# Kernel optimization log

Hardware: AMD Instinct MI355X
Metric: run time of the kernel (lower is better)

The kernel has to match this reference:

```python
import jax, jax.numpy as jnp
import numpy as np

D = 64          # node_hidden_dim
MP_STEPS = 6    # num_step_message_passing
S2S_STEPS = 6   # num_step_set2set
LSTM_LAYERS = 3 # num_layer_set2set


def setup_inputs() -> dict:
    key = jax.random.key(0)
    ks = jax.random.split(key, 32)
    N, E, B = 10000, 50000, 500
    node_in, edge_in, edge_hid, out_dim = 15, 5, 128, 12
    s = 0.1
    inp = {}
    inp["node_feat"] = jax.random.normal(ks[0], (N, node_in), jnp.float32)
    inp["edge_feat"] = jax.random.normal(ks[1], (E, edge_in), jnp.float32)
    inp["src"] = jax.random.randint(ks[2], (E,), 0, N)
    inp["dst"] = jax.random.randint(ks[3], (E,), 0, N)
    inp["graph_ids"] = jnp.sort(jax.random.randint(ks[4], (N,), 0, B))
    inp["num_graphs"] = B
    # lin0
    inp["lin0_W"] = jax.random.normal(ks[5], (node_in, D), jnp.float32) * s
    inp["lin0_b"] = jnp.zeros((D,), jnp.float32)
    # edge network MLP (Linear -> ReLU -> Linear), output reshaped to D x D per edge
    inp["em_W1"] = jax.random.normal(ks[6], (edge_in, edge_hid), jnp.float32) * s
    inp["em_b1"] = jnp.zeros((edge_hid,), jnp.float32)
    inp["em_W2"] = jax.random.normal(ks[7], (edge_hid, D * D), jnp.float32) * 0.02
    inp["em_b2"] = jnp.zeros((D * D,), jnp.float32)
    inp["conv_bias"] = jnp.zeros((D,), jnp.float32)
    # GRU (input D, hidden D), torch layout: [3*D, in], gate order r,z,n
    inp["gru_Wih"] = jax.random.normal(ks[8], (3 * D, D), jnp.float32) * s
    inp["gru_Whh"] = jax.random.normal(ks[9], (3 * D, D), jnp.float32) * s
    inp["gru_bih"] = jnp.zeros((3 * D,), jnp.float32)
    inp["gru_bhh"] = jnp.zeros((3 * D,), jnp.float32)
    # Set2Set LSTM: input 2*D, hidden D, 3 layers. torch layout [4*D, in], gates i,f,g,o
    inp["lstm0_Wih"] = jax.random.normal(ks[10], (4 * D, 2 * D), jnp.float32) * s
    inp["lstm0_Whh"] = jax.random.normal(ks[11], (4 * D, D), jnp.float32) * s
    inp["lstm0_bih"] = jnp.zeros((4 * D,), jnp.float32)
    inp["lstm0_bhh"] = jnp.zeros((4 * D,), jnp.float32)
    inp["lstm12_Wih"] = jax.random.normal(ks[12], (2, 4 * D, D), jnp.float32) * s
    inp["lstm12_Whh"] = jax.random.normal(ks[13], (2, 4 * D, D), jnp.float32) * s
    inp["lstm12_bih"] = jnp.zeros((2, 4 * D), jnp.float32)
    inp["lstm12_bhh"] = jnp.zeros((2, 4 * D), jnp.float32)
    # output head
    inp["lin1_W"] = jax.random.normal(ks[14], (2 * D, D), jnp.float32) * s
    inp["lin1_b"] = jnp.zeros((D,), jnp.float32)
    inp["lin2_W"] = jax.random.normal(ks[15], (D, out_dim), jnp.float32) * s
    inp["lin2_b"] = jnp.zeros((out_dim,), jnp.float32)
    return inp


def _mpnn(node_feat, edge_feat, src, dst, graph_ids, num_graphs,
          lin0_W, lin0_b, em_W1, em_b1, em_W2, em_b2, conv_bias,
          gru_Wih, gru_Whh, gru_bih, gru_bhh,
          lstm0_Wih, lstm0_Whh, lstm0_bih, lstm0_bhh,
          lstm12_Wih, lstm12_Whh, lstm12_bih, lstm12_bhh,
          lin1_W, lin1_b, lin2_W, lin2_b):
    N = node_feat.shape[0]
    E = edge_feat.shape[0]
    B = num_graphs
    # initial node embedding
    out = jax.nn.relu(node_feat @ lin0_W + lin0_b)      # [N, D]
    h = out                                             # GRU hidden (seq_len=1, 1 layer)
    # per-edge weight matrices (edge features are static across steps)
    We = (jax.nn.relu(edge_feat @ em_W1 + em_b1) @ em_W2 + em_b2).reshape(E, D, D)
    for _ in range(MP_STEPS):
        # NNConv: gather src -> per-edge matvec -> scatter-add to dst
        msg = jnp.einsum('ei,eio->eo', out[src], We)    # [E, D]
        agg = jax.ops.segment_sum(msg, dst, num_segments=N) + conv_bias
        m = jax.nn.relu(agg)                            # [N, D]
        # GRU cell (torch gate order r, z, n)
        gx = m @ gru_Wih.T + gru_bih
        gh = h @ gru_Whh.T + gru_bhh
        rx, zx, nx = jnp.split(gx, 3, axis=-1)
        rh, zh, nh = jnp.split(gh, 3, axis=-1)
        r = jax.nn.sigmoid(rx + rh)
        z = jax.nn.sigmoid(zx + zh)
        n = jnp.tanh(nx + r * nh)
        h = (1.0 - z) * n + z * h
        out = h
    # Set2Set readout: 3-layer LSTM over steps, attention over nodes per graph
    h_l = [jnp.zeros((B, D), out.dtype) for _ in range(LSTM_LAYERS)]
    c_l = [jnp.zeros((B, D), out.dtype) for _ in range(LSTM_LAYERS)]
    q_star = jnp.zeros((B, 2 * D), out.dtype)
    for _ in range(S2S_STEPS):
        x = q_star
        for l in range(LSTM_LAYERS):
            if l == 0:
                Wih, Whh, bih, bhh = lstm0_Wih, lstm0_Whh, lstm0_bih, lstm0_bhh
            else:
                Wih, Whh = lstm12_Wih[l - 1], lstm12_Whh[l - 1]
                bih, bhh = lstm12_bih[l - 1], lstm12_bhh[l - 1]
            g = x @ Wih.T + bih + h_l[l] @ Whh.T + bhh
            i_g, f_g, g_g, o_g = jnp.split(g, 4, axis=-1)
            c_l[l] = jax.nn.sigmoid(f_g) * c_l[l] + jax.nn.sigmoid(i_g) * jnp.tanh(g_g)
            h_l[l] = jax.nn.sigmoid(o_g) * jnp.tanh(c_l[l])
            x = h_l[l]
        q = x                                           # [B, D]
        # segment softmax attention
        e = jnp.sum(out * q[graph_ids], axis=-1)        # [N]
        emax = jax.ops.segment_max(e, graph_ids, num_segments=B)
        ex = jnp.exp(e - emax[graph_ids])
        denom = jax.ops.segment_sum(ex, graph_ids, num_segments=B)
        alpha = ex / denom[graph_ids]                   # [N]
        readout = jax.ops.segment_sum(alpha[:, None] * out, graph_ids, num_segments=B)
        q_star = jnp.concatenate([q, readout], axis=-1) # [B, 2D]
    y = jax.nn.relu(q_star @ lin1_W + lin1_b) @ lin2_W + lin2_b
    return y


def reference(node_feat, edge_feat, src, dst, graph_ids, num_graphs,
              lin0_W, lin0_b, em_W1, em_b1, em_W2, em_b2, conv_bias,
              gru_Wih, gru_Whh, gru_bih, gru_bhh,
              lstm0_Wih, lstm0_Whh, lstm0_bih, lstm0_bhh,
              lstm12_Wih, lstm12_Whh, lstm12_bih, lstm12_bhh,
              lin1_W, lin1_b, lin2_W, lin2_b):
    return _mpnn(node_feat, edge_feat, src, dst, graph_ids, num_graphs,
                 lin0_W, lin0_b, em_W1, em_b1, em_W2, em_b2, conv_bias,
                 gru_Wih, gru_Whh, gru_bih, gru_bhh,
                 lstm0_Wih, lstm0_Whh, lstm0_bih, lstm0_bhh,
                 lstm12_Wih, lstm12_Whh, lstm12_bih, lstm12_bhh,
                 lin1_W, lin1_b, lin2_W, lin2_b)
```

## Files before the change

kernel.cpp:

```cpp
#include <hip/hip_runtime.h>
#include <math.h>

#define NGRAPH 500
#define MP_STEPS 6
#define S2S_STEPS 6
#define S2S_CAP 64

typedef _Float16 h8 __attribute__((ext_vector_type(8)));
typedef float f4 __attribute__((ext_vector_type(4)));

__device__ __forceinline__ float sigmoidf_(float v){ return 1.0f/(1.0f + expf(-v)); }

__global__ void k_zero(float* __restrict__ p, int n){
  int i = blockIdx.x*256 + threadIdx.x;
  if(i < n) p[i] = 0.f;
}

__global__ void k_lin0(const float* __restrict__ nf, const float* __restrict__ W,
                       const float* __restrict__ b, float* __restrict__ x, int N){
  int n = blockIdx.x*4 + (threadIdx.x >> 6);
  int d = threadIdx.x & 63;
  if(n >= N) return;
  float acc = b[d];
#pragma unroll
  for(int i=0;i<15;i++) acc = fmaf(nf[n*15+i], W[i*64+d], acc);
  x[n*64+d] = fmaxf(acc, 0.0f);
}

__global__ void k_edgeh(const float* __restrict__ ef, const float* __restrict__ W1,
                        const float* __restrict__ b1, _Float16* __restrict__ he, int E){
  int e = blockIdx.x;
  int h = threadIdx.x;
  if(e >= E || h >= 160) return;
  float v;
  if(h < 128){
    float acc = b1[h];
#pragma unroll
    for(int i=0;i<5;i++) acc = fmaf(ef[e*5+i], W1[i*128+h], acc);
    v = fmaxf(acc, 0.f);
  } else {
    v = (h == 128) ? 1.0f : 0.0f;
  }
  he[(size_t)e*160 + h] = (_Float16)v;
}

__global__ void k_prepW2(const float* __restrict__ W2, const float* __restrict__ b2,
                         _Float16* __restrict__ W2T){
  int idx = blockIdx.x*256 + threadIdx.x;
  if(idx >= 4096*160) return;
  int n = idx / 160, k = idx % 160;
  float v = (k < 128) ? W2[(size_t)k*4096 + n] : ((k == 128) ? b2[n] : 0.f);
  W2T[idx] = (_Float16)v;
}

__global__ __launch_bounds__(512, 2) void k_fmsg(
    const _Float16* __restrict__ he,
    const _Float16* __restrict__ W2T,
    const float* __restrict__ x,
    const int* __restrict__ src, const int* __restrict__ dst,
    float* __restrict__ agg, int E)
{
  __shared__ _Float16 hs[128*160];
  __shared__ float xsT[64*132];
  __shared__ int ds_dst[128];
  const int tid  = threadIdx.x;
  const int wave = tid >> 6;
  const int mrow = wave >> 2;
  const int cg   = wave & 3;
  const int lane = tid & 63;
  const int quad = lane >> 4;
  const int l15  = lane & 15;
  const int e0   = blockIdx.x * 128;

  for(int t = tid; t < 2560; t += 512){
    int r = t / 20, c = t % 20;
    uint4 v = make_uint4(0,0,0,0);
    if(e0 + r < E) v = *(const uint4*)&he[(size_t)(e0+r)*160 + c*8];
    *(uint4*)&hs[r*160 + c*8] = v;
  }
  {
    int j = tid >> 2, qc = tid & 3;
    int sj = (e0 + j < E) ? src[e0 + j] : 0;
    const float4* xr = (const float4*)(x + (size_t)sj*64);
#pragma unroll
    for(int k=0;k<4;k++){
      float4 v = xr[qc*4 + k];
      int ib = qc*16 + k*4;
      xsT[(ib+0)*132 + j] = v.x;
      xsT[(ib+1)*132 + j] = v.y;
      xsT[(ib+2)*132 + j] = v.z;
      xsT[(ib+3)*132 + j] = v.w;
    }
  }
  if(tid < 128) ds_dst[tid] = (e0 + tid < E) ? dst[e0 + tid] : 0;
  __syncthreads();

  h8 af[4][5];
#pragma unroll
  for(int mt=0;mt<4;mt++)
#pragma unroll
    for(int ks=0;ks<5;ks++)
      af[mt][ks] = *(const h8*)&hs[(mrow*64 + mt*16 + l15)*160 + ks*32 + (quad<<3)];

  const _Float16* bbase = W2T + ((size_t)(cg*16 + l15))*160 + (quad<<3);
  h8 bf[5], bn[5];
#pragma unroll
  for(int ks=0;ks<5;ks++) bf[ks] = *(const h8*)(bbase + ks*32);

  f4 macc[4];
#pragma unroll
  for(int mt=0;mt<4;mt++) macc[mt] = (f4){0.f,0.f,0.f,0.f};

#pragma unroll 2
  for(int i=0;i<64;i++){
    if(i < 63){
      const _Float16* nb = bbase + (size_t)(i+1)*64*160;
#pragma unroll
      for(int ks=0;ks<5;ks++) bn[ks] = *(const h8*)(nb + ks*32);
    }
    f4 g0 = (f4){0.f,0.f,0.f,0.f}, g1 = g0, g2 = g0, g3 = g0;
#pragma unroll
    for(int ks=0;ks<5;ks++){
      g0 = __builtin_amdgcn_mfma_f32_16x16x32_f16(af[0][ks], bf[ks], g0, 0, 0, 0);
      g1 = __builtin_amdgcn_mfma_f32_16x16x32_f16(af[1][ks], bf[ks], g1, 0, 0, 0);
      g2 = __builtin_amdgcn_mfma_f32_16x16x32_f16(af[2][ks], bf[ks], g2, 0, 0, 0);
      g3 = __builtin_amdgcn_mfma_f32_16x16x32_f16(af[3][ks], bf[ks], g3, 0, 0, 0);
    }
    f4 xs0 = *(const f4*)&xsT[i*132 + mrow*64 + (quad<<2) +  0];
    f4 xs1 = *(const f4*)&xsT[i*132 + mrow*64 + (quad<<2) + 16];
    f4 xs2 = *(const f4*)&xsT[i*132 + mrow*64 + (quad<<2) + 32];
    f4 xs3 = *(const f4*)&xsT[i*132 + mrow*64 + (quad<<2) + 48];
    macc[0] += xs0 * g0;
    macc[1] += xs1 * g1;
    macc[2] += xs2 * g2;
    macc[3] += xs3 * g3;
#pragma unroll
    for(int ks=0;ks<5;ks++) bf[ks] = bn[ks];
  }

  const int col = cg*16 + l15;
#pragma unroll
  for(int mt=0;mt<4;mt++){
#pragma unroll
    for(int r=0;r<4;r++){
      int edge = mrow*64 + mt*16 + (quad<<2) + r;
      if(e0 + edge < E)
        atomicAdd(&agg[(size_t)ds_dst[edge]*64 + col], macc[mt][r]);
    }
  }
}

__global__ __launch_bounds__(256) void k_gru2(
    float* __restrict__ x, float* __restrict__ agg, const float* __restrict__ cb,
    const float* __restrict__ WihT, const float* __restrict__ WhhT,
    const float* __restrict__ bih, const float* __restrict__ bhh, int N)
{
  __shared__ float ms[32*64], hs2[32*64];
  const int tid = threadIdx.x;
  const int n0 = blockIdx.x*32;
  for(int t=tid; t<2048; t+=256){
    int n = n0 + (t>>6), d = t&63;
    float mv=0.f, hv=0.f;
    if(n < N){
      mv = fmaxf(agg[(size_t)n*64+d] + cb[d], 0.f);
      agg[(size_t)n*64+d] = 0.f;
      hv = x[(size_t)n*64+d];
    }
    ms[t]=mv; hs2[t]=hv;
  }
  __syncthreads();
  const int gx = tid & 31, ng = tid >> 5;
  float ar[4][2]={{0}}, az[4][2]={{0}}, anx[4][2]={{0}}, anh[4][2]={{0}};
#pragma unroll 4
  for(int k=0;k<64;k++){
    float wi0=WihT[k*192+gx],     wi1=WihT[k*192+gx+32];
    float wi2=WihT[k*192+gx+64],  wi3=WihT[k*192+gx+96];
    float wi4=WihT[k*192+gx+128], wi5=WihT[k*192+gx+160];
    float wh0=WhhT[k*192+gx],     wh1=WhhT[k*192+gx+32];
    float wh2=WhhT[k*192+gx+64],  wh3=WhhT[k*192+gx+96];
    float wh4=WhhT[k*192+gx+128], wh5=WhhT[k*192+gx+160];
#pragma unroll
    for(int j=0;j<4;j++){
      float mk = ms[(ng*4+j)*64+k], hk = hs2[(ng*4+j)*64+k];
      ar[j][0] = fmaf(mk,wi0, fmaf(hk,wh0, ar[j][0]));
      ar[j][1] = fmaf(mk,wi1, fmaf(hk,wh1, ar[j][1]));
      az[j][0] = fmaf(mk,wi2, fmaf(hk,wh2, az[j][0]));
      az[j][1] = fmaf(mk,wi3, fmaf(hk,wh3, az[j][1]));
      anx[j][0]= fmaf(mk,wi4, anx[j][0]);
      anx[j][1]= fmaf(mk,wi5, anx[j][1]);
      anh[j][0]= fmaf(hk,wh4, anh[j][0]);
      anh[j][1]= fmaf(hk,wh5, anh[j][1]);
    }
  }
#pragma unroll
  for(int j=0;j<4;j++){
    int n = n0 + ng*4 + j;
    if(n >= N) continue;
#pragma unroll
    for(int c=0;c<2;c++){
      int d = gx + 32*c;
      float r  = sigmoidf_(ar[j][c] + bih[d]     + bhh[d]);
      float z  = sigmoidf_(az[j][c] + bih[64+d]  + bhh[64+d]);
      float nn = tanhf(anx[j][c] + bih[128+d] + r*(anh[j][c] + bhh[128+d]));
      float hv = hs2[(ng*4+j)*64+d];
      x[(size_t)n*64+d] = (1.f - z)*nn + z*hv;
    }
  }
}

__global__ void k_tr_gru(const float* __restrict__ Wih, const float* __restrict__ Whh,
                         float* __restrict__ WihT, float* __restrict__ WhhT){
  int idx = blockIdx.x*256 + threadIdx.x;
  if(idx < 192*64){
    int r = idx/64, i = idx%64;
    WihT[i*192 + r] = Wih[idx];
    WhhT[i*192 + r] = Whh[idx];
  }
}

__global__ void k_tr_lstmcat(const float* __restrict__ w0ih, const float* __restrict__ w0hh,
                             const float* __restrict__ w12ih, const float* __restrict__ w12hh,
                             float* __restrict__ W0cat, float* __restrict__ W12cat){
  int idx = blockIdx.x*256 + threadIdx.x;
  if(idx < 192*256){
    int k = idx / 256, r = idx % 256;
    W0cat[idx] = (k < 128) ? w0ih[r*128 + k] : w0hh[r*64 + (k - 128)];
  }
  if(idx < 2*128*256){
    int l = idx / (128*256);
    int rem = idx % (128*256);
    int k = rem / 256, r = rem % 256;
    W12cat[idx] = (k < 64) ? w12ih[((size_t)l*256 + r)*64 + k]
                           : w12hh[((size_t)l*256 + r)*64 + (k - 64)];
  }
}

__device__ __forceinline__ int lbound(const int* __restrict__ a, int n, int v){
  int lo=0, hi=n;
  while(lo<hi){ int mid=(lo+hi)>>1; if(a[mid]<v) lo=mid+1; else hi=mid; }
  return lo;
}

template<int KTOT>
__device__ __forceinline__ void lstm_layer4(
    float (*__restrict__ qcat)[320], float (*__restrict__ csl)[192],
    int xoff, int hoff, int coff,
    const float* __restrict__ Wcat, const float* __restrict__ bsum,
    f4 (*__restrict__ ps4)[256], int t)
{
  constexpr int CH = KTOT/4;
  const int kc = t >> 6, tq = t & 63;
  const float* wp = Wcat + (size_t)(kc*CH)*256 + 4*tq;
  f4 a0 = (f4){0.f,0.f,0.f,0.f}, a1 = a0, a2 = a0, a3 = a0;
#pragma unroll
  for(int i=0;i<CH;i++){
    f4 w = *(const f4*)(wp + (size_t)i*256);
    int xi = xoff + kc*CH + i;
    a0 += qcat[0][xi] * w;
    a1 += qcat[1][xi] * w;
    a2 += qcat[2][xi] * w;
    a3 += qcat[3][xi] * w;
  }
  ps4[0][t] = a0; ps4[1][t] = a1; ps4[2][t] = a2; ps4[3][t] = a3;
  __syncthreads();
  {
    const int g = t >> 6, d = t & 63;
    float v[4];
#pragma unroll
    for(int gate=0; gate<4; gate++){
      int G = gate*64 + d;
      int q = G >> 2, cmp = G & 3;
      float s = 0.f;
#pragma unroll
      for(int k2=0;k2<4;k2++) s += ps4[g][k2*64 + q][cmp];
      v[gate] = s + bsum[G];
    }
    float ig = sigmoidf_(v[0]);
    float fg = sigmoidf_(v[1]);
    float gg = tanhf(v[2]);
    float og = sigmoidf_(v[3]);
    float cn = fg*csl[g][coff+d] + ig*gg;
    csl[g][coff+d] = cn;
    qcat[g][hoff+d] = og*tanhf(cn);
  }
  __syncthreads();
}

__global__ __launch_bounds__(256) void k_s2s(
    const float* __restrict__ x, const int* __restrict__ gid, int N,
    const float* __restrict__ W0cat, const float* __restrict__ W12cat,
    const float* __restrict__ l0_bih, const float* __restrict__ l0_bhh,
    const float* __restrict__ l12_bih, const float* __restrict__ l12_bhh,
    const float* __restrict__ W1, const float* __restrict__ b1,
    const float* __restrict__ W2, const float* __restrict__ b2,
    float* __restrict__ y)
{
  const int b0 = blockIdx.x * 4;
  const int t = threadIdx.x;
  const int wave = t >> 6, lane = t & 63;
  __shared__ float xt[4][S2S_CAP*65];
  __shared__ float qcat[4][320];
  __shared__ float csl[4][192];
  __shared__ f4    ps4[4][256];
  __shared__ float bsum[768];
  __shared__ int   sh_n0[5];

  if(t < 5) sh_n0[t] = lbound(gid, N, b0 + t);
  for(int i=t; i<4*320; i+=256) ((float*)qcat)[i] = 0.f;
  for(int i=t; i<4*192; i+=256) ((float*)csl)[i] = 0.f;
  for(int i=t; i<768; i+=256){
    int layer = i >> 8, g = i & 255;
    float bi, bh;
    if(layer == 0){ bi = l0_bih[g]; bh = l0_bhh[g]; }
    else { bi = l12_bih[(layer-1)*256+g]; bh = l12_bhh[(layer-1)*256+g]; }
    bsum[i] = bi + bh;
  }
  __syncthreads();
  const int n0w = sh_n0[wave];
  const int cntw = sh_n0[wave+1] - n0w;
  const int ccw = (cntw < S2S_CAP) ? cntw : S2S_CAP;

  for(int j=0;j<ccw;j++)
    xt[wave][j*65 + lane] = x[(size_t)(n0w+j)*64 + lane];
  __syncthreads();

  for(int step=0; step<S2S_STEPS; step++){
    lstm_layer4<192>(qcat, csl,   0, 128,   0, W0cat,          bsum,     ps4, t);
    lstm_layer4<128>(qcat, csl, 128, 192,  64, W12cat,         bsum+256, ps4, t);
    lstm_layer4<128>(qcat, csl, 192, 256, 128, W12cat+128*256, bsum+512, ps4, t);

    const float* q = qcat[wave] + 256;
    float accd = 0.f;
    if(lane < ccw){
      const float* xr = xt[wave] + lane*65;
#pragma unroll 8
      for(int k=0;k<64;k++) accd = fmaf(xr[k], q[k], accd);
    }
    float pm = (lane < ccw) ? accd : -1e30f;
    float qv = q[lane];
    for(int j = S2S_CAP; j < cntw; j++){
      float p = x[(size_t)(n0w+j)*64 + lane] * qv;
#pragma unroll
      for(int o=32;o;o>>=1) p += __shfl_xor(p, o, 64);
      pm = fmaxf(pm, p);
    }
#pragma unroll
    for(int o=32;o;o>>=1) pm = fmaxf(pm, __shfl_xor(pm, o, 64));
    const float mx = pm;

    float ex = (lane < ccw) ? expf(accd - mx) : 0.f;
    float exsum = ex;
#pragma unroll
    for(int o=32;o;o>>=1) exsum += __shfl_xor(exsum, o, 64);

    float racc = 0.f;
    for(int j=0;j<ccw;j++)
      racc = fmaf(__shfl(ex, j, 64), xt[wave][j*65 + lane], racc);
    for(int j = S2S_CAP; j < cntw; j++){
      float xv = x[(size_t)(n0w+j)*64 + lane];
      float p = xv * qv;
#pragma unroll
      for(int o=32;o;o>>=1) p += __shfl_xor(p, o, 64);
      float e2 = expf(p - mx);
      exsum += e2;
      racc = fmaf(e2, xv, racc);
    }
    float inv = (exsum > 0.f) ? 1.f/exsum : 0.f;
    qcat[wave][lane]      = qcat[wave][256 + lane];
    qcat[wave][64 + lane] = racc * inv;
    __syncthreads();
  }
  float* hh = (float*)ps4;
  {
    const int g = t >> 6, d = t & 63;
    float a = b1[d];
#pragma unroll 4
    for(int k=0;k<128;k++) a = fmaf(qcat[g][k], W1[k*64+d], a);
    hh[g*64 + d] = fmaxf(a, 0.f);
  }
  __syncthreads();
  if(t < 48){
    int g = t / 12, o = t % 12;
    float out = b2[o];
#pragma unroll 4
    for(int k=0;k<64;k++) out = fmaf(hh[g*64 + k], W2[k*12+o], out);
    y[(size_t)(b0+g)*12 + o] = out;
  }
}

extern "C" void kernel_launch(void* const* d_in, const int* in_sizes, int n_in,
                              void* d_out, int out_size, void* d_ws, size_t ws_size,
                              hipStream_t stream) {
  const float* node_feat = (const float*)d_in[0];
  const float* edge_feat = (const float*)d_in[1];
  const int*   src       = (const int*)d_in[2];
  const int*   dst       = (const int*)d_in[3];
  const int*   gid       = (const int*)d_in[4];
  const float* lin0_W = (const float*)d_in[6];
  const float* lin0_b = (const float*)d_in[7];
  const float* em_W1  = (const float*)d_in[8];
  const float* em_b1  = (const float*)d_in[9];
  const float* em_W2  = (const float*)d_in[10];
  const float* em_b2  = (const float*)d_in[11];
  const float* conv_b = (const float*)d_in[12];
  const float* gru_Wih = (const float*)d_in[13];
  const float* gru_Whh = (const float*)d_in[14];
  const float* gru_bih = (const float*)d_in[15];
  const float* gru_bhh = (const float*)d_in[16];
  const float* l0_Wih = (const float*)d_in[17];
  const float* l0_Whh = (const float*)d_in[18];
  const float* l0_bih = (const float*)d_in[19];
  const float* l0_bhh = (const float*)d_in[20];
  const float* l12_Wih = (const float*)d_in[21];
  const float* l12_Whh = (const float*)d_in[22];
  const float* l12_bih = (const float*)d_in[23];
  const float* l12_bhh = (const float*)d_in[24];
  const float* lin1_W = (const float*)d_in[25];
  const float* lin1_b = (const float*)d_in[26];
  const float* lin2_W = (const float*)d_in[27];
  const float* lin2_b = (const float*)d_in[28];
  float* y = (float*)d_out;

  const int N = in_sizes[0] / 15;
  const int E = in_sizes[1] / 5;
  const int B = NGRAPH;

  char* p = (char*)d_ws;
  auto carve = [&](size_t bytes)->char* {
    char* r = p; p += (bytes + 255) & ~(size_t)255; return r;
  };
  _Float16* he_h = (_Float16*)carve((size_t)E*160*2);
  _Float16* W2T  = (_Float16*)carve((size_t)4096*160*2);
  float* x      = (float*)carve((size_t)N*64*4);
  float* agg    = (float*)carve((size_t)N*64*4);
  float* gWihT  = (float*)carve(192*64*4);
  float* gWhhT  = (float*)carve(192*64*4);
  float* W0cat  = (float*)carve(192*256*4);
  float* W12cat = (float*)carve(2*128*256*4);
  (void)ws_size; (void)n_in; (void)out_size;

  k_lin0<<<(N+3)/4, 256, 0, stream>>>(node_feat, lin0_W, lin0_b, x, N);
  k_edgeh<<<E, 192, 0, stream>>>(edge_feat, em_W1, em_b1, he_h, E);
  k_prepW2<<<(4096*160+255)/256, 256, 0, stream>>>(em_W2, em_b2, W2T);
  k_tr_gru<<<(192*64+255)/256, 256, 0, stream>>>(gru_Wih, gru_Whh, gWihT, gWhhT);
  k_tr_lstmcat<<<(2*128*256+255)/256, 256, 0, stream>>>(l0_Wih, l0_Whh, l12_Wih, l12_Whh,
                                                        W0cat, W12cat);
  k_zero<<<(N*64+255)/256, 256, 0, stream>>>(agg, N*64);

  const int nblk = (E + 127) / 128;
  for(int s=0; s<MP_STEPS; s++){
    k_fmsg<<<nblk, 512, 0, stream>>>(he_h, W2T, x, src, dst, agg, E);
    k_gru2<<<(N+31)/32, 256, 0, stream>>>(x, agg, conv_b, gWihT, gWhhT, gru_bih, gru_bhh, N);
  }

  k_s2s<<<B/4, 256, 0, stream>>>(x, gid, N,
                                 W0cat, W12cat, l0_bih, l0_bhh,
                                 l12_bih, l12_bhh,
                                 lin1_W, lin1_b, lin2_W, lin2_b, y);
}
```

Measured before the change: 905.7 us.

## Drop bias column from edge GEMM, stream A from swizzled LDS, raise occupancy

The K dimension of the per-edge message GEMM shrinks from 160 to 128. The bias column packed into the hidden features is replaced by adding b2 after the MFMAs. A fragments are no longer held in registers across the loop. They are re-read each iteration from an XOR-swizzled LDS layout meant to avoid bank conflicts, which cuts register pressure enough to request 4 blocks per CU instead of 2. LDS use per block also falls, so more blocks fit. The cost is extra LDS reads inside the inner loop plus a scalar bias load per iteration.

```diff
diff --git a/kernel.cpp b/kernel.cpp
--- a/kernel.cpp
+++ b/kernel.cpp
@@ -31,37 +31,30 @@
                         const float* __restrict__ b1, _Float16* __restrict__ he, int E){
   int e = blockIdx.x;
   int h = threadIdx.x;
-  if(e >= E || h >= 160) return;
-  float v;
-  if(h < 128){
-    float acc = b1[h];
-#pragma unroll
-    for(int i=0;i<5;i++) acc = fmaf(ef[e*5+i], W1[i*128+h], acc);
-    v = fmaxf(acc, 0.f);
-  } else {
-    v = (h == 128) ? 1.0f : 0.0f;
-  }
-  he[(size_t)e*160 + h] = (_Float16)v;
-}
-
-__global__ void k_prepW2(const float* __restrict__ W2, const float* __restrict__ b2,
-                         _Float16* __restrict__ W2T){
+  if(e >= E) return;
+  float acc = b1[h];
+#pragma unroll
+  for(int i=0;i<5;i++) acc = fmaf(ef[e*5+i], W1[i*128+h], acc);
+  he[(size_t)e*128 + h] = (_Float16)fmaxf(acc, 0.f);
+}
+
+__global__ void k_prepW2(const float* __restrict__ W2, _Float16* __restrict__ W2T){
   int idx = blockIdx.x*256 + threadIdx.x;
-  if(idx >= 4096*160) return;
-  int n = idx / 160, k = idx % 160;
-  float v = (k < 128) ? W2[(size_t)k*4096 + n] : ((k == 128) ? b2[n] : 0.f);
-  W2T[idx] = (_Float16)v;
-}
-
-__global__ __launch_bounds__(512, 2) void k_fmsg(
+  if(idx >= 4096*128) return;
+  int n = idx >> 7, k = idx & 127;
+  W2T[idx] = (_Float16)W2[(size_t)k*4096 + n];
+}
+
+__global__ __launch_bounds__(512, 4) void k_fmsg(
     const _Float16* __restrict__ he,
     const _Float16* __restrict__ W2T,
+    const float* __restrict__ b2,
     const float* __restrict__ x,
     const int* __restrict__ src, const int* __restrict__ dst,
     float* __restrict__ agg, int E)
 {
-  __shared__ _Float16 hs[128*160];
-  __shared__ float xsT[64*132];
+  __shared__ _Float16 hs[128*128];
+  __shared__ float xsT[64*128];
   __shared__ int ds_dst[128];
   const int tid  = threadIdx.x;
   const int wave = tid >> 6;
@@ -72,11 +65,11 @@
   const int l15  = lane & 15;
   const int e0   = blockIdx.x * 128;
 
-  for(int t = tid; t < 2560; t += 512){
-    int r = t / 20, c = t % 20;
+  for(int t = tid; t < 2048; t += 512){
+    int r = t >> 4, c = t & 15;
     uint4 v = make_uint4(0,0,0,0);
-    if(e0 + r < E) v = *(const uint4*)&he[(size_t)(e0+r)*160 + c*8];
-    *(uint4*)&hs[r*160 + c*8] = v;
+    if(e0 + r < E) v = *(const uint4*)&he[(size_t)(e0+r)*128 + c*8];
+    *(uint4*)&hs[r*128 + ((c ^ (r&7)) << 3)] = v;
   }
   {
     int j = tid >> 2, qc = tid & 3;
@@ -86,26 +79,30 @@
     for(int k=0;k<4;k++){
       float4 v = xr[qc*4 + k];
       int ib = qc*16 + k*4;
-      xsT[(ib+0)*132 + j] = v.x;
-      xsT[(ib+1)*132 + j] = v.y;
-      xsT[(ib+2)*132 + j] = v.z;
-      xsT[(ib+3)*132 + j] = v.w;
+      xsT[(ib+0)*128 + j] = v.x;
+      xsT[(ib+1)*128 + j] = v.y;
+      xsT[(ib+2)*128 + j] = v.z;
+      xsT[(ib+3)*128 + j] = v.w;
     }
   }
   if(tid < 128) ds_dst[tid] = (e0 + tid < E) ? dst[e0 + tid] : 0;
   __syncthreads();
 
-  h8 af[4][5];
-#pragma unroll
-  for(int mt=0;mt<4;mt++)
-#pragma unroll
-    for(int ks=0;ks<5;ks++)
-      af[mt][ks] = *(const h8*)&hs[(mrow*64 + mt*16 + l15)*160 + ks*32 + (quad<<3)];
-
-  const _Float16* bbase = W2T + ((size_t)(cg*16 + l15))*160 + (quad<<3);
-  h8 bf[5], bn[5];
-#pragma unroll
-  for(int ks=0;ks<5;ks++) bf[ks] = *(const h8*)(bbase + ks*32);
+  const int l7 = l15 & 7;
+  const int qp = quad ^ (l7 & 3);
+  const int hp = l7 >> 2;
+  const int oA = ((hp << 2) | qp) << 4;
+  const int oB = (((1 ^ hp) << 2) | qp) << 4;
+  unsigned a0 = (unsigned)((mrow*64 + l15) << 8) + oA;
+  unsigned a1 = (unsigned)((mrow*64 + l15) << 8) + oB;
+  const char* hsb = (const char*)hs;
+
+  const int col = cg*16 + l15;
+  const _Float16* bbase = W2T + ((size_t)col)*128 + (quad<<3);
+  h8 bf[4], bn[4];
+#pragma unroll
+  for(int ks=0;ks<4;ks++) bf[ks] = *(const h8*)(bbase + ks*32);
+  float b2f = b2[col], b2n = 0.f;
 
   f4 macc[4];
 #pragma unroll
@@ -114,31 +111,39 @@
 #pragma unroll 2
   for(int i=0;i<64;i++){
     if(i < 63){
-      const _Float16* nb = bbase + (size_t)(i+1)*64*160;
-#pragma unroll
-      for(int ks=0;ks<5;ks++) bn[ks] = *(const h8*)(nb + ks*32);
+      const _Float16* nb = bbase + (size_t)(i+1)*8192;
+#pragma unroll
+      for(int ks=0;ks<4;ks++) bn[ks] = *(const h8*)(nb + ks*32);
+      b2n = b2[(i+1)*64 + col];
     }
     f4 g0 = (f4){0.f,0.f,0.f,0.f}, g1 = g0, g2 = g0, g3 = g0;
 #pragma unroll
-    for(int ks=0;ks<5;ks++){
-      g0 = __builtin_amdgcn_mfma_f32_16x16x32_f16(af[0][ks], bf[ks], g0, 0, 0, 0);
-      g1 = __builtin_amdgcn_mfma_f32_16x16x32_f16(af[1][ks], bf[ks], g1, 0, 0, 0);
-      g2 = __builtin_amdgcn_mfma_f32_16x16x32_f16(af[2][ks], bf[ks], g2, 0, 0, 0);
-      g3 = __builtin_amdgcn_mfma_f32_16x16x32_f16(af[3][ks], bf[ks], g3, 0, 0, 0);
-    }
-    f4 xs0 = *(const f4*)&xsT[i*132 + mrow*64 + (quad<<2) +  0];
-    f4 xs1 = *(const f4*)&xsT[i*132 + mrow*64 + (quad<<2) + 16];
-    f4 xs2 = *(const f4*)&xsT[i*132 + mrow*64 + (quad<<2) + 32];
-    f4 xs3 = *(const f4*)&xsT[i*132 + mrow*64 + (quad<<2) + 48];
+    for(int mt=0;mt<4;mt++){
+      h8 A0 = *(const h8*)(hsb + a0 + mt*4096);
+      h8 A1 = *(const h8*)(hsb + a1 + mt*4096);
+      h8 A2 = *(const h8*)(hsb + a0 + mt*4096 + 128);
+      h8 A3 = *(const h8*)(hsb + a1 + mt*4096 + 128);
+      f4* g = (mt==0)?&g0:(mt==1)?&g1:(mt==2)?&g2:&g3;
+      *g = __builtin_amdgcn_mfma_f32_16x16x32_f16(A0, bf[0], *g, 0, 0, 0);
+      *g = __builtin_amdgcn_mfma_f32_16x16x32_f16(A1, bf[1], *g, 0, 0, 0);
+      *g = __builtin_amdgcn_mfma_f32_16x16x32_f16(A2, bf[2], *g, 0, 0, 0);
+      *g = __builtin_amdgcn_mfma_f32_16x16x32_f16(A3, bf[3], *g, 0, 0, 0);
+    }
+    g0 += b2f; g1 += b2f; g2 += b2f; g3 += b2f;
+    f4 xs0 = *(const f4*)&xsT[i*128 + mrow*64 +  0 + (quad<<2)];
+    f4 xs1 = *(const f4*)&xsT[i*128 + mrow*64 + 16 + (quad<<2)];
+    f4 xs2 = *(const f4*)&xsT[i*128 + mrow*64 + 32 + (quad<<2)];
+    f4 xs3 = *(const f4*)&xsT[i*128 + mrow*64 + 48 + (quad<<2)];
     macc[0] += xs0 * g0;
     macc[1] += xs1 * g1;
     macc[2] += xs2 * g2;
     macc[3] += xs3 * g3;
 #pragma unroll
-    for(int ks=0;ks<5;ks++) bf[ks] = bn[ks];
-  }
-
-  const int col = cg*16 + l15;
+    for(int ks=0;ks<4;ks++) bf[ks] = bn[ks];
+    b2f = b2n;
+    asm volatile("" : "+v"(a0), "+v"(a1));
+  }
+
 #pragma unroll
   for(int mt=0;mt<4;mt++){
 #pragma unroll
@@ -429,8 +434,8 @@
   auto carve = [&](size_t bytes)->char* {
     char* r = p; p += (bytes + 255) & ~(size_t)255; return r;
   };
-  _Float16* he_h = (_Float16*)carve((size_t)E*160*2);
-  _Float16* W2T  = (_Float16*)carve((size_t)4096*160*2);
+  _Float16* he_h = (_Float16*)carve((size_t)E*128*2);
+  _Float16* W2T  = (_Float16*)carve((size_t)4096*128*2);
   float* x      = (float*)carve((size_t)N*64*4);
   float* agg    = (float*)carve((size_t)N*64*4);
   float* gWihT  = (float*)carve(192*64*4);
@@ -440,8 +445,8 @@
   (void)ws_size; (void)n_in; (void)out_size;
 
   k_lin0<<<(N+3)/4, 256, 0, stream>>>(node_feat, lin0_W, lin0_b, x, N);
-  k_edgeh<<<E, 192, 0, stream>>>(edge_feat, em_W1, em_b1, he_h, E);
-  k_prepW2<<<(4096*160+255)/256, 256, 0, stream>>>(em_W2, em_b2, W2T);
+  k_edgeh<<<E, 128, 0, stream>>>(edge_feat, em_W1, em_b1, he_h, E);
+  k_prepW2<<<(4096*128+255)/256, 256, 0, stream>>>(em_W2, W2T);
   k_tr_gru<<<(192*64+255)/256, 256, 0, stream>>>(gru_Wih, gru_Whh, gWihT, gWhhT);
   k_tr_lstmcat<<<(2*128*256+255)/256, 256, 0, stream>>>(l0_Wih, l0_Whh, l12_Wih, l12_Whh,
                                                         W0cat, W12cat);
@@ -449,7 +454,7 @@
 
   const int nblk = (E + 127) / 128;
   for(int s=0; s<MP_STEPS; s++){
-    k_fmsg<<<nblk, 512, 0, stream>>>(he_h, W2T, x, src, dst, agg, E);
+    k_fmsg<<<nblk, 512, 0, stream>>>(he_h, W2T, em_b2, x, src, dst, agg, E);
     k_gru2<<<(N+31)/32, 256, 0, stream>>>(x, agg, conv_b, gWihT, gWhhT, gru_bih, gru_bhh, N);
   }
 
```

Result: slower. 1.082 ms (+19.5%).
